# Performance work log

Hardware: AMD Instinct MI355X
Metric: run time of the kernel (lower is better)

## Reference

```python
import jax, jax.numpy as jnp
import numpy as np

B, S, D = 2, 2048, 1024
H = 16
HD = D // H  # 64


def _xavier(key, shape):
    fan_in, fan_out = shape[1], shape[0]
    a = jnp.sqrt(6.0 / (fan_in + fan_out))
    return jax.random.uniform(key, shape, jnp.float32, -a, a)


def setup_inputs() -> dict:
    key = jax.random.key(0)
    ks = jax.random.split(key, 7)
    xq = jax.random.normal(ks[0], (B, S, D), jnp.float32)
    xv = jax.random.normal(ks[1], (B, S, D), jnp.float32)
    xk = jax.random.normal(ks[2], (B, S, D), jnp.float32)
    Wq = _xavier(ks[3], (D, D)); bq = jnp.zeros((D,), jnp.float32)
    Wk = _xavier(ks[4], (D, D)); bk = jnp.zeros((D,), jnp.float32)
    Wv = _xavier(ks[5], (D, D)); bv = jnp.zeros((D,), jnp.float32)
    Wo = _xavier(ks[6], (D, D)); bo = jnp.zeros((D,), jnp.float32)
    return {"xq": xq, "xv": xv, "xk": xk,
            "Wq": Wq, "bq": bq, "Wk": Wk, "bk": bk,
            "Wv": Wv, "bv": bv, "Wo": Wo, "bo": bo}


def reference(xq, xv, xk, Wq, bq, Wk, bk, Wv, bv, Wo, bo):
    # Q/K/V projections (torch Linear: x @ W.T + b), split heads -> [B,H,S,HD]
    q = (xq @ Wq.T + bq).reshape(B, S, H, HD).transpose(0, 2, 1, 3)
    k = (xk @ Wk.T + bk).reshape(B, S, H, HD).transpose(0, 2, 1, 3)
    v = (xv @ Wv.T + bv).reshape(B, S, H, HD).transpose(0, 2, 1, 3)
    # scaled dot-product attention, no mask
    logits = jnp.einsum('bhqd,bhkd->bhqk', q, k) / jnp.sqrt(jnp.float32(HD))
    attn = jax.nn.softmax(logits, axis=-1)
    values = jnp.einsum('bhqk,bhkd->bhqd', attn, v)
    values = values.transpose(0, 2, 1, 3).reshape(B, S, D)
    return values @ Wo.T + bo
```

## Files before the change

kernel.cpp:

```cpp
#include <hip/hip_runtime.h>

typedef __bf16 bf16x8 __attribute__((ext_vector_type(8)));
typedef float f32x4 __attribute__((ext_vector_type(4)));
typedef __attribute__((address_space(1))) const unsigned char ga_t;
typedef __attribute__((address_space(3))) unsigned char la_t;

static __device__ __forceinline__ unsigned short f2b(float f) {
  union { float f; unsigned int i; } c; c.f = f;
  unsigned int r = c.i + 0x7FFFu + ((c.i >> 16) & 1u);
  return (unsigned short)(r >> 16);
}
static __device__ __forceinline__ unsigned int pack2(float a, float b) {
  return (unsigned int)f2b(a) | ((unsigned int)f2b(b) << 16);
}
static __device__ __forceinline__ int4 ld8f_cvt(const float* __restrict__ p) {
  float4 a = *(const float4*)p;
  float4 b = *(const float4*)(p + 4);
  unsigned short u[8];
  u[0] = f2b(a.x); u[1] = f2b(a.y); u[2] = f2b(a.z); u[3] = f2b(a.w);
  u[4] = f2b(b.x); u[5] = f2b(b.y); u[6] = f2b(b.z); u[7] = f2b(b.w);
  return *(int4*)u;
}
static __device__ __forceinline__ void glds16(const unsigned short* g, unsigned short* l) {
  __builtin_amdgcn_global_load_lds((ga_t*)g, (la_t*)l, 16, 0, 0);
}

__global__ __launch_bounds__(256)
void cvt_z(const float* __restrict__ s0, const float* __restrict__ s1,
           const float* __restrict__ s2, const float* __restrict__ s3,
           unsigned short* d0, unsigned short* d1,
           unsigned short* d2, unsigned short* d3, int n8) {
  const int z = blockIdx.y;
  const float* s = z == 0 ? s0 : z == 1 ? s1 : z == 2 ? s2 : s3;
  unsigned short* d = z == 0 ? d0 : z == 1 ? d1 : z == 2 ? d2 : d3;
  int idx = blockIdx.x * 256 + threadIdx.x;
  if (idx < n8) *(int4*)(d + (size_t)idx * 8) = ld8f_cvt(s + (size_t)idx * 8);
}

static __device__ __forceinline__ void gemm_core(
    const unsigned short* __restrict__ A, const unsigned short* __restrict__ W,
    unsigned short* sA, unsigned short* sB, f32x4 acc[4][4],
    int K, int m0, int n0) {
  const int tid = threadIdx.x;
  const int wave = tid >> 6, lane = tid & 63, quad = lane >> 4, l16 = lane & 15;
  const int wrow = (wave >> 1) * 64, wcol = (wave & 1) * 64;
  const int r = tid >> 2, c8 = (tid & 3) * 8;

  const unsigned short* gA0 = A + (size_t)(m0 + r) * K + c8;
  const unsigned short* gA1 = gA0 + (size_t)64 * K;
  const unsigned short* gB0 = W + (size_t)(n0 + r) * K + c8;
  const unsigned short* gB1 = gB0 + (size_t)64 * K;
  unsigned short* lA0 = sA + tid * 8;
  unsigned short* lA1 = lA0 + 2048;
  unsigned short* lB0 = sB + tid * 8;
  unsigned short* lB1 = lB0 + 2048;

  for (int k0 = 0; k0 < K; k0 += 32) {
    __syncthreads();
    glds16(gA0 + k0, lA0);
    glds16(gA1 + k0, lA1);
    glds16(gB0 + k0, lB0);
    glds16(gB1 + k0, lB1);
    __syncthreads();

    bf16x8 af[4], bfv[4];
#pragma unroll
    for (int i = 0; i < 4; ++i)
      af[i] = *(const bf16x8*)(&sA[(wrow + i * 16 + l16) * 32 + quad * 8]);
#pragma unroll
    for (int j = 0; j < 4; ++j)
      bfv[j] = *(const bf16x8*)(&sB[(wcol + j * 16 + l16) * 32 + quad * 8]);
#pragma unroll
    for (int i = 0; i < 4; ++i)
#pragma unroll
      for (int j = 0; j < 4; ++j)
        acc[i][j] = __builtin_amdgcn_mfma_f32_16x16x32_bf16(af[i], bfv[j], acc[i][j], 0, 0, 0);
  }
}

__global__ __launch_bounds__(256, 3)
void gemm_qkv(const unsigned short* __restrict__ A0p, const unsigned short* __restrict__ A1p,
              const unsigned short* __restrict__ A2p,
              const unsigned short* __restrict__ W0p, const unsigned short* __restrict__ W1p,
              const unsigned short* __restrict__ W2p,
              const float* __restrict__ b0p, const float* __restrict__ b1p,
              const float* __restrict__ b2p,
              unsigned short* __restrict__ C0p, unsigned short* __restrict__ C1p,
              unsigned short* __restrict__ C2p,
              int M, int N, int K, int zbase) {
  __shared__ __align__(16) unsigned short smem[8192];
  const int z = blockIdx.z + zbase;
  const unsigned short* A = z == 0 ? A0p : z == 1 ? A1p : A2p;
  const unsigned short* W = z == 0 ? W0p : z == 1 ? W1p : W2p;
  const float* bias = z == 0 ? b0p : z == 1 ? b1p : b2p;

  const int tid = threadIdx.x;
  const int wave = tid >> 6, lane = tid & 63, quad = lane >> 4, l16 = lane & 15;
  const int m0 = blockIdx.x * 128, n0 = blockIdx.y * 128;
  const int wrow = (wave >> 1) * 64, wcol = (wave & 1) * 64;

  f32x4 acc[4][4];
#pragma unroll
  for (int i = 0; i < 4; ++i)
#pragma unroll
    for (int j = 0; j < 4; ++j) acc[i][j] = (f32x4){0.f, 0.f, 0.f, 0.f};

  gemm_core(A, W, smem, smem + 4096, acc, K, m0, n0);

  if (z < 2) {
    unsigned short* C = z == 0 ? C0p : C1p;
#pragma unroll
    for (int j = 0; j < 4; ++j) {
      const int col = n0 + wcol + j * 16 + l16;
      const float bv = bias[col];
#pragma unroll
      for (int i = 0; i < 4; ++i)
#pragma unroll
        for (int r = 0; r < 4; ++r) {
          const int row = m0 + wrow + i * 16 + quad * 4 + r;
          C[(size_t)row * N + col] = f2b(acc[i][j][r] + bv);
        }
    }
  } else {
    __syncthreads();
    unsigned short* sT = smem + wave * 1152;
#pragma unroll
    for (int j = 0; j < 4; ++j) {
      const float bv = bias[n0 + wcol + j * 16 + l16];
#pragma unroll
      for (int i = 0; i < 4; ++i) {
        uint2 pk;
        pk.x = pack2(acc[i][j][0] + bv, acc[i][j][1] + bv);
        pk.y = pack2(acc[i][j][2] + bv, acc[i][j][3] + bv);
        *(uint2*)(&sT[l16 * 72 + i * 16 + quad * 4]) = pk;
      }
#pragma unroll
      for (int t = 0; t < 2; ++t) {
        const int nl = lane >> 2;
        const int colh = (lane & 3) * 8 + t * 32;
        int4 v = *(const int4*)(&sT[nl * 72 + colh]);
        *(int4*)(&C2p[(size_t)(n0 + wcol + j * 16 + nl) * M + m0 + wrow + colh]) = v;
      }
    }
  }
}

__global__ __launch_bounds__(256, 3)
void gemm_out(const unsigned short* __restrict__ A, const unsigned short* __restrict__ W,
              const float* __restrict__ bias, float* __restrict__ C,
              int M, int N, int K) {
  __shared__ __align__(16) unsigned short smem[8192];
  const int tid = threadIdx.x;
  const int wave = tid >> 6, lane = tid & 63, quad = lane >> 4, l16 = lane & 15;
  const int m0 = blockIdx.x * 128, n0 = blockIdx.y * 128;
  const int wrow = (wave >> 1) * 64, wcol = (wave & 1) * 64;

  f32x4 acc[4][4];
#pragma unroll
  for (int i = 0; i < 4; ++i)
#pragma unroll
    for (int j = 0; j < 4; ++j) acc[i][j] = (f32x4){0.f, 0.f, 0.f, 0.f};

  gemm_core(A, W, smem, smem + 4096, acc, K, m0, n0);

#pragma unroll
  for (int j = 0; j < 4; ++j) {
    const int col = n0 + wcol + j * 16 + l16;
    const float bv = bias[col];
#pragma unroll
    for (int i = 0; i < 4; ++i)
#pragma unroll
      for (int r = 0; r < 4; ++r) {
        const int row = m0 + wrow + i * 16 + quad * 4 + r;
        C[(size_t)row * N + col] = acc[i][j][r] + bv;
      }
  }
}

#define SEQ 2048
#define DMODEL 1024

__global__ __launch_bounds__(256, 2)
void attn_fused(const unsigned short* __restrict__ Q,
                const unsigned short* __restrict__ Km,
                const unsigned short* __restrict__ Vt,
                unsigned short* __restrict__ O) {
  __shared__ __align__(16) unsigned short sQ[128 * 72];
  __shared__ __align__(16) unsigned short sK[64 * 72];
  __shared__ __align__(16) unsigned short sVt[64 * 72];
  __shared__ __align__(16) unsigned short sP[4][32 * 72];

  const int tid = threadIdx.x;
  const int wave = tid >> 6, lane = tid & 63, quad = lane >> 4, l16 = lane & 15;
  const int qt = blockIdx.x;
  const int bh = blockIdx.y;
  const int b = bh >> 4, h = bh & 15;
  const size_t qrow0 = (size_t)b * SEQ + qt * 128;
  const size_t kvrow0 = (size_t)b * SEQ;
  const int hcol = h * 64;
  const int bofs = b * SEQ;

#pragma unroll
  for (int i = 0; i < 4; ++i) {
    const int idx = tid + i * 256;
    const int r = idx >> 3, c = (idx & 7) * 8;
    *(int4*)(&sQ[r * 72 + c]) = *(const int4*)(&Q[(qrow0 + r) * DMODEL + hcol + c]);
  }
  __syncthreads();

  const int qw = wave * 32;
  bf16x8 qa[2][2];
#pragma unroll
  for (int qi = 0; qi < 2; ++qi)
#pragma unroll
    for (int ks = 0; ks < 2; ++ks)
      qa[qi][ks] = *(const bf16x8*)(&sQ[(qw + qi * 16 + l16) * 72 + ks * 32 + quad * 8]);

  f32x4 acc[2][4];
#pragma unroll
  for (int qi = 0; qi < 2; ++qi)
#pragma unroll
    for (int hg = 0; hg < 4; ++hg) acc[qi][hg] = (f32x4){0.f, 0.f, 0.f, 0.f};
  float lsum[2] = {0.f, 0.f};

  const float SCL = 0.18033688011112042f;
  const int sr = tid >> 3, sc = (tid & 7) * 8;

  for (int kt = 0; kt < SEQ; kt += 64) {
    __syncthreads();
    {
      const int idx2 = tid + 256;
      const int r2 = idx2 >> 3, c2 = (idx2 & 7) * 8;
      *(int4*)(&sK[sr * 72 + sc]) = *(const int4*)(&Km[(kvrow0 + kt + sr) * DMODEL + hcol + sc]);
      *(int4*)(&sK[r2 * 72 + c2]) = *(const int4*)(&Km[(kvrow0 + kt + r2) * DMODEL + hcol + c2]);
      *(int4*)(&sVt[sr * 72 + sc]) = *(const int4*)(&Vt[(size_t)(hcol + sr) * 4096 + bofs + kt + sc]);
      *(int4*)(&sVt[r2 * 72 + c2]) = *(const int4*)(&Vt[(size_t)(hcol + r2) * 4096 + bofs + kt + c2]);
    }
    __syncthreads();

    f32x4 s[2][4];
#pragma unroll
    for (int qi = 0; qi < 2; ++qi)
#pragma unroll
      for (int kg = 0; kg < 4; ++kg) s[qi][kg] = (f32x4){0.f, 0.f, 0.f, 0.f};
#pragma unroll
    for (int kg = 0; kg < 4; ++kg) {
      bf16x8 kb0 = *(const bf16x8*)(&sK[(kg * 16 + l16) * 72 + quad * 8]);
      bf16x8 kb1 = *(const bf16x8*)(&sK[(kg * 16 + l16) * 72 + 32 + quad * 8]);
#pragma unroll
      for (int qi = 0; qi < 2; ++qi) {
        s[qi][kg] = __builtin_amdgcn_mfma_f32_16x16x32_bf16(kb0, qa[qi][0], s[qi][kg], 0, 0, 0);
        s[qi][kg] = __builtin_amdgcn_mfma_f32_16x16x32_bf16(kb1, qa[qi][1], s[qi][kg], 0, 0, 0);
      }
    }

#pragma unroll
    for (int qi = 0; qi < 2; ++qi)
#pragma unroll
      for (int kg = 0; kg < 4; ++kg) {
        float p0 = __builtin_amdgcn_exp2f(s[qi][kg][0] * SCL);
        float p1 = __builtin_amdgcn_exp2f(s[qi][kg][1] * SCL);
        float p2 = __builtin_amdgcn_exp2f(s[qi][kg][2] * SCL);
        float p3 = __builtin_amdgcn_exp2f(s[qi][kg][3] * SCL);
        lsum[qi] += (p0 + p1) + (p2 + p3);
        uint2 pk; pk.x = pack2(p0, p1); pk.y = pack2(p2, p3);
        *(uint2*)(&sP[wave][(qi * 16 + l16) * 72 + kg * 16 + quad * 4]) = pk;
      }

#pragma unroll
    for (int ks = 0; ks < 2; ++ks) {
      bf16x8 pa[2], vb[4];
#pragma unroll
      for (int qi = 0; qi < 2; ++qi)
        pa[qi] = *(const bf16x8*)(&sP[wave][(qi * 16 + l16) * 72 + ks * 32 + quad * 8]);
#pragma unroll
      for (int hg = 0; hg < 4; ++hg)
        vb[hg] = *(const bf16x8*)(&sVt[(hg * 16 + l16) * 72 + ks * 32 + quad * 8]);
#pragma unroll
      for (int qi = 0; qi < 2; ++qi)
#pragma unroll
        for (int hg = 0; hg < 4; ++hg)
          acc[qi][hg] = __builtin_amdgcn_mfma_f32_16x16x32_bf16(pa[qi], vb[hg], acc[qi][hg], 0, 0, 0);
    }
  }

  float linv[2][4];
#pragma unroll
  for (int qi = 0; qi < 2; ++qi) {
    float v = lsum[qi];
    v += __shfl_xor(v, 16, 64);
    v += __shfl_xor(v, 32, 64);
    lsum[qi] = v;
  }
#pragma unroll
  for (int qi = 0; qi < 2; ++qi)
#pragma unroll
    for (int r = 0; r < 4; ++r)
      linv[qi][r] = 1.0f / __shfl(lsum[qi], quad * 4 + r, 64);

#pragma unroll
  for (int qi = 0; qi < 2; ++qi)
#pragma unroll
    for (int hg = 0; hg < 4; ++hg)
#pragma unroll
      for (int r = 0; r < 4; ++r) {
        const size_t row = qrow0 + qw + qi * 16 + quad * 4 + r;
        O[row * DMODEL + hcol + hg * 16 + l16] = f2b(acc[qi][hg][r] * linv[qi][r]);
      }
}

extern "C" void kernel_launch(void* const* d_in, const int* in_sizes, int n_in,
                              void* d_out, int out_size, void* d_ws, size_t ws_size,
                              hipStream_t stream) {
  const float* xq = (const float*)d_in[0];
  const float* xv = (const float*)d_in[1];
  const float* xk = (const float*)d_in[2];
  const float* Wq = (const float*)d_in[3];
  const float* bq = (const float*)d_in[4];
  const float* Wk = (const float*)d_in[5];
  const float* bk = (const float*)d_in[6];
  const float* Wv = (const float*)d_in[7];
  const float* bv = (const float*)d_in[8];
  const float* Wo = (const float*)d_in[9];
  const float* bo = (const float*)d_in[10];
  float* out = (float*)d_out;

  const int S = 2048, D = 1024, M = 4096;
  const size_t MD = (size_t)M * D, DD = (size_t)D * D;
  unsigned short* P = (unsigned short*)d_ws;
  dim3 bb(256);
  dim3 gg(M / 128, D / 128);

  const size_t need = (3 * MD + 4 * DD + 3 * MD) * 2;
  if (ws_size >= need) {
    unsigned short* Ab = P;
    unsigned short* Wb = Ab + 3 * MD;
    unsigned short* Qw = Wb + 4 * DD;
    unsigned short* Kw = Qw + MD;
    unsigned short* Vtw = Kw + MD;
    unsigned short* Ao = Ab;

    cvt_z<<<dim3((int)(MD / 8 / 256), 3), bb, 0, stream>>>(
        xq, xk, xv, xq, Ab, Ab + MD, Ab + 2 * MD, Ab, (int)(MD / 8));
    cvt_z<<<dim3((int)(DD / 8 / 256), 4), bb, 0, stream>>>(
        Wq, Wk, Wv, Wo, Wb, Wb + DD, Wb + 2 * DD, Wb + 3 * DD, (int)(DD / 8));
    gemm_qkv<<<dim3(M / 128, D / 128, 3), bb, 0, stream>>>(
        Ab, Ab + MD, Ab + 2 * MD, Wb, Wb + DD, Wb + 2 * DD,
        bq, bk, bv, Qw, Kw, Vtw, M, D, D, 0);
    attn_fused<<<dim3(S / 128, 32), bb, 0, stream>>>(Qw, Kw, Vtw, Ao);
    gemm_out<<<gg, bb, 0, stream>>>(Ao, Wb + 3 * DD, bo, out, M, D, D);
  } else {
    unsigned short* Ab = P;
    unsigned short* Wb = Ab + MD;
    unsigned short* Qw = Wb + DD;
    unsigned short* Kw = Qw + MD;
    unsigned short* Vtw = Kw + MD;
    unsigned short* Ao = Ab;
    const int an = (int)(MD / 8), wn = (int)(DD / 8);

    cvt_z<<<dim3(an / 256, 1), bb, 0, stream>>>(xq, xq, xq, xq, Ab, Ab, Ab, Ab, an);
    cvt_z<<<dim3(wn / 256, 1), bb, 0, stream>>>(Wq, Wq, Wq, Wq, Wb, Wb, Wb, Wb, wn);
    gemm_qkv<<<dim3(M / 128, D / 128, 1), bb, 0, stream>>>(
        Ab, Ab, Ab, Wb, Wb, Wb, bq, bq, bq, Qw, Qw, Qw, M, D, D, 0);

    cvt_z<<<dim3(an / 256, 1), bb, 0, stream>>>(xk, xk, xk, xk, Ab, Ab, Ab, Ab, an);
    cvt_z<<<dim3(wn / 256, 1), bb, 0, stream>>>(Wk, Wk, Wk, Wk, Wb, Wb, Wb, Wb, wn);
    gemm_qkv<<<dim3(M / 128, D / 128, 1), bb, 0, stream>>>(
        Ab, Ab, Ab, Wb, Wb, Wb, bk, bk, bk, Kw, Kw, Kw, M, D, D, 0);

    cvt_z<<<dim3(an / 256, 1), bb, 0, stream>>>(xv, xv, xv, xv, Ab, Ab, Ab, Ab, an);
    cvt_z<<<dim3(wn / 256, 1), bb, 0, stream>>>(Wv, Wv, Wv, Wv, Wb, Wb, Wb, Wb, wn);
    gemm_qkv<<<dim3(M / 128, D / 128, 1), bb, 0, stream>>>(
        Ab, Ab, Ab, Wb, Wb, Wb, bv, bv, bv, Vtw, Vtw, Vtw, M, D, D, 2);

    attn_fused<<<dim3(S / 128, 32), bb, 0, stream>>>(Qw, Kw, Vtw, Ao);

    cvt_z<<<dim3(wn / 256, 1), bb, 0, stream>>>(Wo, Wo, Wo, Wo, Wb, Wb, Wb, Wb, wn);
    gemm_out<<<gg, bb, 0, stream>>>(Ao, Wb, bo, out, M, D, D);
  }
}
```

Before: 236.5 us.

## Restructure attention kernel to two waves with 64 query rows each and register prefetch

The attention kernel now runs 128 threads per block, and each wave owns 64 query rows instead of 32, which doubles the reuse of K and V tile fragments per LDS read. Q is loaded straight from global memory into registers, so the shared Q buffer and its barrier are gone. The next K/V tile is prefetched into registers while the current one is being computed, overlapping global loads with MFMA work. The P scratch buffer gets a padded stride of 88, and the score work is split into two 32-key halves to limit register pressure. The cost is more registers per thread and fewer threads per block, which may reduce occupancy or latency hiding.

```diff
diff --git a/kernel.cpp b/kernel.cpp
--- a/kernel.cpp
+++ b/kernel.cpp
@@ -180,132 +180,138 @@
 #define SEQ 2048
 #define DMODEL 1024
 
-__global__ __launch_bounds__(256, 2)
+__global__ __launch_bounds__(128, 2)
 void attn_fused(const unsigned short* __restrict__ Q,
                 const unsigned short* __restrict__ Km,
                 const unsigned short* __restrict__ Vt,
                 unsigned short* __restrict__ O) {
-  __shared__ __align__(16) unsigned short sQ[128 * 72];
   __shared__ __align__(16) unsigned short sK[64 * 72];
   __shared__ __align__(16) unsigned short sVt[64 * 72];
-  __shared__ __align__(16) unsigned short sP[4][32 * 72];
+  __shared__ __align__(16) unsigned short sP[2][64 * 88];
 
   const int tid = threadIdx.x;
   const int wave = tid >> 6, lane = tid & 63, quad = lane >> 4, l16 = lane & 15;
   const int qt = blockIdx.x;
   const int bh = blockIdx.y;
   const int b = bh >> 4, h = bh & 15;
-  const size_t qrow0 = (size_t)b * SEQ + qt * 128;
+  const size_t qrow0 = (size_t)b * SEQ + qt * 128 + wave * 64;
   const size_t kvrow0 = (size_t)b * SEQ;
   const int hcol = h * 64;
   const int bofs = b * SEQ;
 
+  bf16x8 qa[4][2];
+#pragma unroll
+  for (int qg = 0; qg < 4; ++qg)
+#pragma unroll
+    for (int ks = 0; ks < 2; ++ks) {
+      int4 v = *(const int4*)(&Q[(qrow0 + qg * 16 + l16) * DMODEL + hcol + ks * 32 + quad * 8]);
+      qa[qg][ks] = *(bf16x8*)&v;
+    }
+
+  f32x4 acc[4][4];
+#pragma unroll
+  for (int qg = 0; qg < 4; ++qg)
+#pragma unroll
+    for (int hg = 0; hg < 4; ++hg) acc[qg][hg] = (f32x4){0.f, 0.f, 0.f, 0.f};
+  float lsum[4] = {0.f, 0.f, 0.f, 0.f};
+
+  const float SCL = 0.18033688011112042f;
+
+  const int srow = tid >> 3, scol = (tid & 7) * 8;
+
+  int4 kpre[4], vpre[4];
 #pragma unroll
   for (int i = 0; i < 4; ++i) {
-    const int idx = tid + i * 256;
-    const int r = idx >> 3, c = (idx & 7) * 8;
-    *(int4*)(&sQ[r * 72 + c]) = *(const int4*)(&Q[(qrow0 + r) * DMODEL + hcol + c]);
-  }
-  __syncthreads();
-
-  const int qw = wave * 32;
-  bf16x8 qa[2][2];
-#pragma unroll
-  for (int qi = 0; qi < 2; ++qi)
-#pragma unroll
-    for (int ks = 0; ks < 2; ++ks)
-      qa[qi][ks] = *(const bf16x8*)(&sQ[(qw + qi * 16 + l16) * 72 + ks * 32 + quad * 8]);
-
-  f32x4 acc[2][4];
-#pragma unroll
-  for (int qi = 0; qi < 2; ++qi)
-#pragma unroll
-    for (int hg = 0; hg < 4; ++hg) acc[qi][hg] = (f32x4){0.f, 0.f, 0.f, 0.f};
-  float lsum[2] = {0.f, 0.f};
-
-  const float SCL = 0.18033688011112042f;
-  const int sr = tid >> 3, sc = (tid & 7) * 8;
+    const int rr = srow + i * 16;
+    kpre[i] = *(const int4*)(&Km[(kvrow0 + rr) * DMODEL + hcol + scol]);
+    vpre[i] = *(const int4*)(&Vt[(size_t)(hcol + rr) * 4096 + bofs + scol]);
+  }
 
   for (int kt = 0; kt < SEQ; kt += 64) {
     __syncthreads();
-    {
-      const int idx2 = tid + 256;
-      const int r2 = idx2 >> 3, c2 = (idx2 & 7) * 8;
-      *(int4*)(&sK[sr * 72 + sc]) = *(const int4*)(&Km[(kvrow0 + kt + sr) * DMODEL + hcol + sc]);
-      *(int4*)(&sK[r2 * 72 + c2]) = *(const int4*)(&Km[(kvrow0 + kt + r2) * DMODEL + hcol + c2]);
-      *(int4*)(&sVt[sr * 72 + sc]) = *(const int4*)(&Vt[(size_t)(hcol + sr) * 4096 + bofs + kt + sc]);
-      *(int4*)(&sVt[r2 * 72 + c2]) = *(const int4*)(&Vt[(size_t)(hcol + r2) * 4096 + bofs + kt + c2]);
-    }
-    __syncthreads();
-
-    f32x4 s[2][4];
-#pragma unroll
-    for (int qi = 0; qi < 2; ++qi)
-#pragma unroll
-      for (int kg = 0; kg < 4; ++kg) s[qi][kg] = (f32x4){0.f, 0.f, 0.f, 0.f};
-#pragma unroll
-    for (int kg = 0; kg < 4; ++kg) {
-      bf16x8 kb0 = *(const bf16x8*)(&sK[(kg * 16 + l16) * 72 + quad * 8]);
-      bf16x8 kb1 = *(const bf16x8*)(&sK[(kg * 16 + l16) * 72 + 32 + quad * 8]);
-#pragma unroll
-      for (int qi = 0; qi < 2; ++qi) {
-        s[qi][kg] = __builtin_amdgcn_mfma_f32_16x16x32_bf16(kb0, qa[qi][0], s[qi][kg], 0, 0, 0);
-        s[qi][kg] = __builtin_amdgcn_mfma_f32_16x16x32_bf16(kb1, qa[qi][1], s[qi][kg], 0, 0, 0);
-      }
-    }
-
-#pragma unroll
-    for (int qi = 0; qi < 2; ++qi)
-#pragma unroll
-      for (int kg = 0; kg < 4; ++kg) {
-        float p0 = __builtin_amdgcn_exp2f(s[qi][kg][0] * SCL);
-        float p1 = __builtin_amdgcn_exp2f(s[qi][kg][1] * SCL);
-        float p2 = __builtin_amdgcn_exp2f(s[qi][kg][2] * SCL);
-        float p3 = __builtin_amdgcn_exp2f(s[qi][kg][3] * SCL);
-        lsum[qi] += (p0 + p1) + (p2 + p3);
-        uint2 pk; pk.x = pack2(p0, p1); pk.y = pack2(p2, p3);
-        *(uint2*)(&sP[wave][(qi * 16 + l16) * 72 + kg * 16 + quad * 4]) = pk;
-      }
-
-#pragma unroll
-    for (int ks = 0; ks < 2; ++ks) {
-      bf16x8 pa[2], vb[4];
-#pragma unroll
-      for (int qi = 0; qi < 2; ++qi)
-        pa[qi] = *(const bf16x8*)(&sP[wave][(qi * 16 + l16) * 72 + ks * 32 + quad * 8]);
+#pragma unroll
+    for (int i = 0; i < 4; ++i) {
+      const int rr = srow + i * 16;
+      *(int4*)(&sK[rr * 72 + scol]) = kpre[i];
+      *(int4*)(&sVt[rr * 72 + scol]) = vpre[i];
+    }
+    __syncthreads();
+
+    const int ktn = (kt + 64 < SEQ) ? kt + 64 : kt;
+#pragma unroll
+    for (int i = 0; i < 4; ++i) {
+      const int rr = srow + i * 16;
+      kpre[i] = *(const int4*)(&Km[(kvrow0 + ktn + rr) * DMODEL + hcol + scol]);
+      vpre[i] = *(const int4*)(&Vt[(size_t)(hcol + rr) * 4096 + bofs + ktn + scol]);
+    }
+
+#pragma unroll
+    for (int kh = 0; kh < 2; ++kh) {
+      f32x4 s[4][2];
+#pragma unroll
+      for (int qg = 0; qg < 4; ++qg)
+#pragma unroll
+        for (int kg = 0; kg < 2; ++kg) s[qg][kg] = (f32x4){0.f, 0.f, 0.f, 0.f};
+#pragma unroll
+      for (int kg = 0; kg < 2; ++kg) {
+        const int key16 = kh * 2 + kg;
+        bf16x8 kb0 = *(const bf16x8*)(&sK[(key16 * 16 + l16) * 72 + quad * 8]);
+        bf16x8 kb1 = *(const bf16x8*)(&sK[(key16 * 16 + l16) * 72 + 32 + quad * 8]);
+#pragma unroll
+        for (int qg = 0; qg < 4; ++qg) {
+          s[qg][kg] = __builtin_amdgcn_mfma_f32_16x16x32_bf16(kb0, qa[qg][0], s[qg][kg], 0, 0, 0);
+          s[qg][kg] = __builtin_amdgcn_mfma_f32_16x16x32_bf16(kb1, qa[qg][1], s[qg][kg], 0, 0, 0);
+        }
+      }
+#pragma unroll
+      for (int qg = 0; qg < 4; ++qg)
+#pragma unroll
+        for (int kg = 0; kg < 2; ++kg) {
+          float p0 = __builtin_amdgcn_exp2f(s[qg][kg][0] * SCL);
+          float p1 = __builtin_amdgcn_exp2f(s[qg][kg][1] * SCL);
+          float p2 = __builtin_amdgcn_exp2f(s[qg][kg][2] * SCL);
+          float p3 = __builtin_amdgcn_exp2f(s[qg][kg][3] * SCL);
+          lsum[qg] += (p0 + p1) + (p2 + p3);
+          uint2 pk; pk.x = pack2(p0, p1); pk.y = pack2(p2, p3);
+          *(uint2*)(&sP[wave][(qg * 16 + l16) * 88 + (kh * 2 + kg) * 16 + quad * 4]) = pk;
+        }
+      bf16x8 paf[4], vbf[4];
+#pragma unroll
+      for (int qg = 0; qg < 4; ++qg)
+        paf[qg] = *(const bf16x8*)(&sP[wave][(qg * 16 + l16) * 88 + kh * 32 + quad * 8]);
 #pragma unroll
       for (int hg = 0; hg < 4; ++hg)
-        vb[hg] = *(const bf16x8*)(&sVt[(hg * 16 + l16) * 72 + ks * 32 + quad * 8]);
-#pragma unroll
-      for (int qi = 0; qi < 2; ++qi)
+        vbf[hg] = *(const bf16x8*)(&sVt[(hg * 16 + l16) * 72 + kh * 32 + quad * 8]);
+#pragma unroll
+      for (int qg = 0; qg < 4; ++qg)
 #pragma unroll
         for (int hg = 0; hg < 4; ++hg)
-          acc[qi][hg] = __builtin_amdgcn_mfma_f32_16x16x32_bf16(pa[qi], vb[hg], acc[qi][hg], 0, 0, 0);
-    }
-  }
-
-  float linv[2][4];
-#pragma unroll
-  for (int qi = 0; qi < 2; ++qi) {
-    float v = lsum[qi];
+          acc[qg][hg] = __builtin_amdgcn_mfma_f32_16x16x32_bf16(paf[qg], vbf[hg], acc[qg][hg], 0, 0, 0);
+    }
+  }
+
+  float linv[4][4];
+#pragma unroll
+  for (int qg = 0; qg < 4; ++qg) {
+    float v = lsum[qg];
     v += __shfl_xor(v, 16, 64);
     v += __shfl_xor(v, 32, 64);
-    lsum[qi] = v;
-  }
-#pragma unroll
-  for (int qi = 0; qi < 2; ++qi)
+    lsum[qg] = v;
+  }
+#pragma unroll
+  for (int qg = 0; qg < 4; ++qg)
 #pragma unroll
     for (int r = 0; r < 4; ++r)
-      linv[qi][r] = 1.0f / __shfl(lsum[qi], quad * 4 + r, 64);
-
-#pragma unroll
-  for (int qi = 0; qi < 2; ++qi)
+      linv[qg][r] = 1.0f / __shfl(lsum[qg], quad * 4 + r, 64);
+
+#pragma unroll
+  for (int qg = 0; qg < 4; ++qg)
 #pragma unroll
     for (int hg = 0; hg < 4; ++hg)
 #pragma unroll
       for (int r = 0; r < 4; ++r) {
-        const size_t row = qrow0 + qw + qi * 16 + quad * 4 + r;
-        O[row * DMODEL + hcol + hg * 16 + l16] = f2b(acc[qi][hg][r] * linv[qi][r]);
+        const size_t row = qrow0 + qg * 16 + quad * 4 + r;
+        O[row * DMODEL + hcol + hg * 16 + l16] = f2b(acc[qg][hg][r] * linv[qg][r]);
       }
 }
 
@@ -347,7 +353,7 @@
     gemm_qkv<<<dim3(M / 128, D / 128, 3), bb, 0, stream>>>(
         Ab, Ab + MD, Ab + 2 * MD, Wb, Wb + DD, Wb + 2 * DD,
         bq, bk, bv, Qw, Kw, Vtw, M, D, D, 0);
-    attn_fused<<<dim3(S / 128, 32), bb, 0, stream>>>(Qw, Kw, Vtw, Ao);
+    attn_fused<<<dim3(S / 128, 32), dim3(128), 0, stream>>>(Qw, Kw, Vtw, Ao);
     gemm_out<<<gg, bb, 0, stream>>>(Ao, Wb + 3 * DD, bo, out, M, D, D);
   } else {
     unsigned short* Ab = P;
@@ -373,7 +379,7 @@
     gemm_qkv<<<dim3(M / 128, D / 128, 1), bb, 0, stream>>>(
         Ab, Ab, Ab, Wb, Wb, Wb, bv, bv, bv, Vtw, Vtw, Vtw, M, D, D, 2);
 
-    attn_fused<<<dim3(S / 128, 32), bb, 0, stream>>>(Qw, Kw, Vtw, Ao);
+    attn_fused<<<dim3(S / 128, 32), dim3(128), 0, stream>>>(Qw, Kw, Vtw, Ao);
 
     cvt_z<<<dim3(wn / 256, 1), bb, 0, stream>>>(Wo, Wo, Wo, Wo, Wb, Wb, Wb, Wb, wn);
     gemm_out<<<gg, bb, 0, stream>>>(Ao, Wb, bo, out, M, D, D);
```

After: 295.2 us. +24.8%, slower.
